# Kernel optimization log

Hardware: AMD Instinct MI355X
Metric: run time of the kernel (lower is better)

The kernel has to match this reference:

```python
import jax, jax.numpy as jnp
import numpy as np
from jax import lax

MARGIN = 0.2
NMAX = 1


def setup_inputs() -> dict:
    key = jax.random.key(0)
    k1, k2 = jax.random.split(key)
    N, D = 8192, 512
    imgs = jax.random.normal(k1, (N, D), dtype=jnp.float32)
    caps = jax.random.normal(k2, (N, D), dtype=jnp.float32)
    return {"imgs": imgs, "caps": caps}


def reference(imgs, caps):
    # scores[i, j] = <img_i, cap_j>  -> [N, N]
    scores = jnp.matmul(imgs, caps.T)
    diag = jnp.diagonal(scores)  # [N]
    s = scores - 2.0 * jnp.diag(diag)
    # top-nmax over columns (axis 0): hardest negative captions per caption slot
    max_c = lax.top_k(s.T, NMAX)[0].T  # [NMAX, N]
    # top-nmax over rows (axis 1): hardest negative images per image slot
    max_i = lax.top_k(s, NMAX)[0]      # [N, NMAX]
    neg_cap = jnp.sum(jnp.maximum(max_c + (MARGIN - diag)[None, :], 0.0))
    neg_img = jnp.sum(jnp.maximum(max_i + (MARGIN - diag)[:, None], 0.0))
    return neg_cap + neg_img
```

## Files before the change

### kernel.cpp

```cpp
#include <hip/hip_runtime.h>

#define N_ROWS 8192
#define DIM    512

typedef __attribute__((ext_vector_type(4))) float frag_cd;
typedef __attribute__((ext_vector_type(2))) long long v2ll;

__device__ __forceinline__ unsigned f2fp8(float x) {
    float a = fabsf(x);
    unsigned s = (__float_as_uint(x) >> 31) << 7;
    if (a < 0.015625f) return s;
    a = fminf(a, 448.f);
    unsigned u = __float_as_uint(a);
    u += 0x7FFFFu + ((u >> 20) & 1u);
    unsigned exp = (u >> 23) - 120u;
    unsigned mant = (u >> 20) & 7u;
    return s | (exp << 3) | mant;
}
__device__ __forceinline__ unsigned pack4fp8(float4 v) {
    return f2fp8(v.x) | (f2fp8(v.y) << 8) | (f2fp8(v.z) << 16) | (f2fp8(v.w) << 24);
}
__device__ __forceinline__ unsigned enc_f32(float f) {
    unsigned u = __float_as_uint(f);
    return (u & 0x80000000u) ? ~u : (u | 0x80000000u);
}
__device__ __forceinline__ float dec_f32(unsigned k) {
    return __uint_as_float((k & 0x80000000u) ? (k & 0x7FFFFFFFu) : ~k);
}


__global__ __launch_bounds__(256) void k_prep(const float* __restrict__ imgs,
                                              const float* __restrict__ caps,
                                              unsigned char* __restrict__ fimgs,
                                              unsigned char* __restrict__ fcaps,
                                              float* __restrict__ diag,
                                              unsigned* __restrict__ rowmax,
                                              unsigned* __restrict__ colmax,
                                              float* __restrict__ out) {
    const int cr = blockIdx.x;
    const int t  = threadIdx.x;
    const int w = t >> 6, l = t & 63;
    const int kp = l >> 3, cg = l & 3, par = (l >> 2) & 1;
    if (cr == 0 && t == 0) out[0] = 0.f;
    const size_t ubase = (size_t)cr * 8192 + kp * 1024 + cg * 256 + par * 8;
    float ps[4];
    #pragma unroll
    for (int i = 0; i < 4; ++i) {
        const int row = w + 4 * i;
        const float* ar = imgs + ((size_t)cr * 16 + row) * DIM + l * 8;
        const float* br = caps + ((size_t)cr * 16 + row) * DIM + l * 8;
        float4 a0 = *(const float4*)ar, a1 = *(const float4*)(ar + 4);
        float4 b0 = *(const float4*)br, b1 = *(const float4*)(br + 4);
        uint2 oa, ob;
        oa.x = pack4fp8(a0); oa.y = pack4fp8(a1);
        ob.x = pack4fp8(b0); ob.y = pack4fp8(b1);
        *(uint2*)(fimgs + ubase + row * 16) = oa;
        *(uint2*)(fcaps + ubase + row * 16) = ob;
        ps[i] = a0.x * b0.x + a0.y * b0.y + a0.z * b0.z + a0.w * b0.w
              + a1.x * b1.x + a1.y * b1.y + a1.z * b1.z + a1.w * b1.w;
    }
    #pragma unroll
    for (int i = 0; i < 4; ++i) {
        float s = ps[i];
        #pragma unroll
        for (int m = 1; m < 64; m <<= 1) s += __shfl_xor(s, m, 64);
        if (l == 0) {
            const int r = cr * 16 + w + 4 * i;
            diag[r] = s; rowmax[r] = 0u; colmax[r] = 0u;
        }
    }
}

__global__ __launch_bounds__(256, 6) void k_gemm(const unsigned char* __restrict__ A,
                                                 const unsigned char* __restrict__ B,
                                                 unsigned* __restrict__ rowmax,
                                                 unsigned* __restrict__ colmax) {
    __shared__ unsigned char sA[2][4096];
    __shared__ unsigned char sB[2][8192];
    const int tid = threadIdx.x;
    const int w = tid >> 6, lane = tid & 63;
    const int f = (int)blockIdx.x;
    const int jb = (f & 7) * 8 + ((f >> 3) & 7);
    const int ib = f >> 6;
    const int j0 = jb << 7, i0 = ib << 6;
    const int q = lane >> 4, l15 = lane & 15;
    const int wr = (w & 1) << 5, wc = (w >> 1) << 6;

    const unsigned char* Ab = A + (size_t)(i0 >> 4) * 8192 + lane * 16;
    const unsigned char* Bb = B + (size_t)(j0 >> 4) * 8192 + lane * 16;

    frag_cd acc[2][4] = {};

    auto stage = [&](int bi, int kp) {
        __builtin_amdgcn_global_load_lds(
            (const __attribute__((address_space(1))) unsigned int*)(Ab + (size_t)w * 8192 + kp * 1024),
            (__attribute__((address_space(3))) unsigned int*)(&sA[bi][(w << 10) + (lane << 4)]), 16, 0, 0);
        #pragma unroll
        for (int j = 0; j < 2; ++j) {
            const int s = 2 * w + j;
            __builtin_amdgcn_global_load_lds(
                (const __attribute__((address_space(1))) unsigned int*)(Bb + (size_t)s * 8192 + kp * 1024),
                (__attribute__((address_space(3))) unsigned int*)(&sB[bi][(s << 10) + (lane << 4)]), 16, 0, 0);
        }
    };

    stage(0, 0);
    __syncthreads();

    const int u16 = ((q << 4) + l15) << 4;

    #pragma unroll
    for (int kp = 0; kp < 8; ++kp) {
        const int cur = kp & 1, nxt = cur ^ 1;
        if (kp < 7) stage(nxt, kp + 1);

        v2ll af[2], bfr[4];
        #pragma unroll
        for (int r = 0; r < 2; ++r)
            af[r] = *(const v2ll*)(&sA[cur][((((w & 1) << 1) + r) << 10) + u16]);
        #pragma unroll
        for (int c = 0; c < 4; ++c)
            bfr[c] = *(const v2ll*)(&sB[cur][((((w >> 1) << 2) + c) << 10) + u16]);
        #pragma unroll
        for (int r = 0; r < 2; ++r)
            #pragma unroll
            for (int c = 0; c < 4; ++c)
                acc[r][c] = __builtin_amdgcn_mfma_f32_16x16x32_fp8_fp8(af[r][0], bfr[c][0], acc[r][c], 0, 0, 0);
        #pragma unroll
        for (int r = 0; r < 2; ++r)
            #pragma unroll
            for (int c = 0; c < 4; ++c)
                acc[r][c] = __builtin_amdgcn_mfma_f32_16x16x32_fp8_fp8(af[r][1], bfr[c][1], acc[r][c], 0, 0, 0);

        __syncthreads();
    }

    const bool dblk = ((i0 >> 7) == jb);
    #pragma unroll
    for (int r = 0; r < 2; ++r)
        #pragma unroll
        for (int c = 0; c < 4; ++c)
            #pragma unroll
            for (int g = 0; g < 4; ++g) {
                float fv = acc[r][c][g];
                const int gi = wr + (r << 4) + (q << 2) + g;
                const int gj = wc + (c << 4) + l15;
                if (dblk && (i0 + gi) == (j0 + gj)) fv = -fv;
                acc[r][c][g] = fv;
            }

    #pragma unroll
    for (int r = 0; r < 2; ++r)
        #pragma unroll
        for (int g = 0; g < 4; ++g) {
            float m = fmaxf(fmaxf(acc[r][0][g], acc[r][1][g]),
                            fmaxf(acc[r][2][g], acc[r][3][g]));
            m = fmaxf(m, __shfl_xor(m, 1, 64));
            m = fmaxf(m, __shfl_xor(m, 2, 64));
            m = fmaxf(m, __shfl_xor(m, 4, 64));
            m = fmaxf(m, __shfl_xor(m, 8, 64));
            if (l15 == 0)
                atomicMax(&rowmax[i0 + wr + (r << 4) + (q << 2) + g], enc_f32(m));
        }
    #pragma unroll
    for (int c = 0; c < 4; ++c) {
        float m = acc[0][c][0];
        #pragma unroll
        for (int r = 0; r < 2; ++r)
            #pragma unroll
            for (int g = 0; g < 4; ++g) m = fmaxf(m, acc[r][c][g]);
        m = fmaxf(m, __shfl_xor(m, 16, 64));
        m = fmaxf(m, __shfl_xor(m, 32, 64));
        if (q == 0)
            atomicMax(&colmax[j0 + wc + (c << 4) + l15], enc_f32(m));
    }
}

__global__ __launch_bounds__(256) void k_final(const unsigned* __restrict__ rowmax,
                                               const unsigned* __restrict__ colmax,
                                               const float* __restrict__ diag,
                                               float* __restrict__ out) {
    const int idx = blockIdx.x * 256 + threadIdx.x;
    const float d = diag[idx];
    float s = fmaxf(dec_f32(rowmax[idx]) + 0.2f - d, 0.f)
            + fmaxf(dec_f32(colmax[idx]) + 0.2f - d, 0.f);
    #pragma unroll
    for (int m = 1; m < 64; m <<= 1) s += __shfl_xor(s, m, 64);
    __shared__ float red[4];
    if ((threadIdx.x & 63) == 0) red[threadIdx.x >> 6] = s;
    __syncthreads();
    if (threadIdx.x == 0)
        atomicAdd(out, red[0] + red[1] + red[2] + red[3]);
}

extern "C" void kernel_launch(void* const* d_in, const int* in_sizes, int n_in,
                              void* d_out, int out_size, void* d_ws, size_t ws_size,
                              hipStream_t stream) {
    const float* imgs = (const float*)d_in[0];
    const float* caps = (const float*)d_in[1];
    float* out = (float*)d_out;

    char* ws = (char*)d_ws;
    unsigned char* fimgs = (unsigned char*)ws;
    unsigned char* fcaps = (unsigned char*)(ws + 4194304);
    float*    diag   = (float*)   (ws + 8388608);
    unsigned* rowmax = (unsigned*)(ws + 8388608 + 32768);
    unsigned* colmax = (unsigned*)(ws + 8388608 + 65536);

    k_prep<<<N_ROWS / 16, 256, 0, stream>>>(imgs, caps, fimgs, fcaps,
                                            diag, rowmax, colmax, out);
    k_gemm<<<8192, 256, 0, stream>>>(fimgs, fcaps, rowmax, colmax);
    k_final<<<N_ROWS / 256, 256, 0, stream>>>(rowmax, colmax, diag, out);
}
```

Baseline: 159.6 us.

## Switch FP8 GEMM to 16x16x128 scaled MFMA with matching operand layout

Replaces pairs of 16x16x32 fp8 MFMAs with the gfx950 16x16x128 f8f6f4 scaled MFMA using unit scales, so each step now covers 128 K. The prep kernel is rewritten to emit a packed layout matching the wider operand fragments, and it launches more blocks, each converting fewer rows. The GEMM stages double-sized LDS tiles over four K steps instead of eight, with the occupancy hint lowered to match the larger shared memory. The aims are fewer MFMA issues and sync points; the costs are more LDS per block and a likely drop in occupancy.

```diff
diff --git a/kernel.cpp b/kernel.cpp
--- a/kernel.cpp
+++ b/kernel.cpp
@@ -4,7 +4,8 @@
 #define DIM    512
 
 typedef __attribute__((ext_vector_type(4))) float frag_cd;
-typedef __attribute__((ext_vector_type(2))) long long v2ll;
+typedef __attribute__((ext_vector_type(4))) int   v4i;
+typedef __attribute__((ext_vector_type(8))) int   v8i;
 
 __device__ __forceinline__ unsigned f2fp8(float x) {
     float a = fabsf(x);
@@ -37,46 +38,38 @@
                                               unsigned* __restrict__ rowmax,
                                               unsigned* __restrict__ colmax,
                                               float* __restrict__ out) {
-    const int cr = blockIdx.x;
+    const int b  = blockIdx.x;
+    const int cr = b >> 2;
     const int t  = threadIdx.x;
     const int w = t >> 6, l = t & 63;
-    const int kp = l >> 3, cg = l & 3, par = (l >> 2) & 1;
-    if (cr == 0 && t == 0) out[0] = 0.f;
-    const size_t ubase = (size_t)cr * 8192 + kp * 1024 + cg * 256 + par * 8;
-    float ps[4];
-    #pragma unroll
-    for (int i = 0; i < 4; ++i) {
-        const int row = w + 4 * i;
-        const float* ar = imgs + ((size_t)cr * 16 + row) * DIM + l * 8;
-        const float* br = caps + ((size_t)cr * 16 + row) * DIM + l * 8;
-        float4 a0 = *(const float4*)ar, a1 = *(const float4*)(ar + 4);
-        float4 b0 = *(const float4*)br, b1 = *(const float4*)(br + 4);
-        uint2 oa, ob;
-        oa.x = pack4fp8(a0); oa.y = pack4fp8(a1);
-        ob.x = pack4fp8(b0); ob.y = pack4fp8(b1);
-        *(uint2*)(fimgs + ubase + row * 16) = oa;
-        *(uint2*)(fcaps + ubase + row * 16) = ob;
-        ps[i] = a0.x * b0.x + a0.y * b0.y + a0.z * b0.z + a0.w * b0.w
-              + a1.x * b1.x + a1.y * b1.y + a1.z * b1.z + a1.w * b1.w;
-    }
-    #pragma unroll
-    for (int i = 0; i < 4; ++i) {
-        float s = ps[i];
-        #pragma unroll
-        for (int m = 1; m < 64; m <<= 1) s += __shfl_xor(s, m, 64);
-        if (l == 0) {
-            const int r = cr * 16 + w + 4 * i;
-            diag[r] = s; rowmax[r] = 0u; colmax[r] = 0u;
-        }
-    }
-}
-
-__global__ __launch_bounds__(256, 6) void k_gemm(const unsigned char* __restrict__ A,
+    const int row = ((b & 3) << 2) + w;
+    if (b == 0 && t == 0) out[0] = 0.f;
+    const int r = cr * 16 + row;
+    const float* ar = imgs + (size_t)r * DIM + l * 8;
+    const float* br = caps + (size_t)r * DIM + l * 8;
+    float4 a0 = *(const float4*)ar, a1 = *(const float4*)(ar + 4);
+    float4 b0 = *(const float4*)br, b1 = *(const float4*)(br + 4);
+    uint2 oa, ob;
+    oa.x = pack4fp8(a0); oa.y = pack4fp8(a1);
+    ob.x = pack4fp8(b0); ob.y = pack4fp8(b1);
+    const size_t addr = (size_t)cr * 8192 + (size_t)((l >> 4) << 11)
+                      + (((l >> 1) & 1) << 10)
+                      + ((((l >> 2) & 3) << 4) + row) * 16 + ((l & 1) << 3);
+    *(uint2*)(fimgs + addr) = oa;
+    *(uint2*)(fcaps + addr) = ob;
+    float s = a0.x * b0.x + a0.y * b0.y + a0.z * b0.z + a0.w * b0.w
+            + a1.x * b1.x + a1.y * b1.y + a1.z * b1.z + a1.w * b1.w;
+    #pragma unroll
+    for (int m = 1; m < 64; m <<= 1) s += __shfl_xor(s, m, 64);
+    if (l == 0) { diag[r] = s; rowmax[r] = 0u; colmax[r] = 0u; }
+}
+
+__global__ __launch_bounds__(256, 3) void k_gemm(const unsigned char* __restrict__ A,
                                                  const unsigned char* __restrict__ B,
                                                  unsigned* __restrict__ rowmax,
                                                  unsigned* __restrict__ colmax) {
-    __shared__ unsigned char sA[2][4096];
-    __shared__ unsigned char sB[2][8192];
+    __shared__ unsigned char sA[2][8192];
+    __shared__ unsigned char sB[2][16384];
     const int tid = threadIdx.x;
     const int w = tid >> 6, lane = tid & 63;
     const int f = (int)blockIdx.x;
@@ -91,46 +84,61 @@
 
     frag_cd acc[2][4] = {};
 
-    auto stage = [&](int bi, int kp) {
-        __builtin_amdgcn_global_load_lds(
-            (const __attribute__((address_space(1))) unsigned int*)(Ab + (size_t)w * 8192 + kp * 1024),
-            (__attribute__((address_space(3))) unsigned int*)(&sA[bi][(w << 10) + (lane << 4)]), 16, 0, 0);
-        #pragma unroll
-        for (int j = 0; j < 2; ++j) {
-            const int s = 2 * w + j;
+    auto stage = [&](int bi, int kp2) {
+        #pragma unroll
+        for (int j = 0; j < 2; ++j)
             __builtin_amdgcn_global_load_lds(
-                (const __attribute__((address_space(1))) unsigned int*)(Bb + (size_t)s * 8192 + kp * 1024),
-                (__attribute__((address_space(3))) unsigned int*)(&sB[bi][(s << 10) + (lane << 4)]), 16, 0, 0);
+                (const __attribute__((address_space(1))) unsigned int*)(Ab + (size_t)w * 8192 + kp2 * 2048 + j * 1024),
+                (__attribute__((address_space(3))) unsigned int*)(&sA[bi][(w << 11) + (j << 10) + (lane << 4)]), 16, 0, 0);
+        #pragma unroll
+        for (int s = 0; s < 2; ++s) {
+            const int ch = 2 * w + s;
+            #pragma unroll
+            for (int j = 0; j < 2; ++j)
+                __builtin_amdgcn_global_load_lds(
+                    (const __attribute__((address_space(1))) unsigned int*)(Bb + (size_t)ch * 8192 + kp2 * 2048 + j * 1024),
+                    (__attribute__((address_space(3))) unsigned int*)(&sB[bi][(ch << 11) + (j << 10) + (lane << 4)]), 16, 0, 0);
         }
     };
 
     stage(0, 0);
     __syncthreads();
 
-    const int u16 = ((q << 4) + l15) << 4;
-
-    #pragma unroll
-    for (int kp = 0; kp < 8; ++kp) {
-        const int cur = kp & 1, nxt = cur ^ 1;
-        if (kp < 7) stage(nxt, kp + 1);
-
-        v2ll af[2], bfr[4];
+    const int u16 = lane << 4;
+
+    #pragma unroll
+    for (int kp2 = 0; kp2 < 4; ++kp2) {
+        const int cur = kp2 & 1, nxt = cur ^ 1;
+        if (kp2 < 3) stage(nxt, kp2 + 1);
+
+        v8i af[2], bf[4];
+        #pragma unroll
+        for (int r = 0; r < 2; ++r) {
+            const int ch = ((w & 1) << 1) + r;
+            v4i lo = *(const v4i*)(&sA[cur][(ch << 11) + u16]);
+            v4i hi = *(const v4i*)(&sA[cur][(ch << 11) + 1024 + u16]);
+            v8i v;
+            v[0] = lo[0]; v[1] = lo[1]; v[2] = lo[2]; v[3] = lo[3];
+            v[4] = hi[0]; v[5] = hi[1]; v[6] = hi[2]; v[7] = hi[3];
+            af[r] = v;
+        }
+        #pragma unroll
+        for (int c = 0; c < 4; ++c) {
+            const int ch = ((w >> 1) << 2) + c;
+            v4i lo = *(const v4i*)(&sB[cur][(ch << 11) + u16]);
+            v4i hi = *(const v4i*)(&sB[cur][(ch << 11) + 1024 + u16]);
+            v8i v;
+            v[0] = lo[0]; v[1] = lo[1]; v[2] = lo[2]; v[3] = lo[3];
+            v[4] = hi[0]; v[5] = hi[1]; v[6] = hi[2]; v[7] = hi[3];
+            bf[c] = v;
+        }
         #pragma unroll
         for (int r = 0; r < 2; ++r)
-            af[r] = *(const v2ll*)(&sA[cur][((((w & 1) << 1) + r) << 10) + u16]);
-        #pragma unroll
-        for (int c = 0; c < 4; ++c)
-            bfr[c] = *(const v2ll*)(&sB[cur][((((w >> 1) << 2) + c) << 10) + u16]);
-        #pragma unroll
-        for (int r = 0; r < 2; ++r)
             #pragma unroll
             for (int c = 0; c < 4; ++c)
-                acc[r][c] = __builtin_amdgcn_mfma_f32_16x16x32_fp8_fp8(af[r][0], bfr[c][0], acc[r][c], 0, 0, 0);
-        #pragma unroll
-        for (int r = 0; r < 2; ++r)
-            #pragma unroll
-            for (int c = 0; c < 4; ++c)
-                acc[r][c] = __builtin_amdgcn_mfma_f32_16x16x32_fp8_fp8(af[r][1], bfr[c][1], acc[r][c], 0, 0, 0);
+                acc[r][c] = __builtin_amdgcn_mfma_scale_f32_16x16x128_f8f6f4(
+                    af[r], bf[c], acc[r][c], 0, 0,
+                    0, 0x7F7F7F7F, 0, 0x7F7F7F7F);
 
         __syncthreads();
     }
@@ -207,8 +215,8 @@
     unsigned* rowmax = (unsigned*)(ws + 8388608 + 32768);
     unsigned* colmax = (unsigned*)(ws + 8388608 + 65536);
 
-    k_prep<<<N_ROWS / 16, 256, 0, stream>>>(imgs, caps, fimgs, fcaps,
-                                            diag, rowmax, colmax, out);
+    k_prep<<<2048, 256, 0, stream>>>(imgs, caps, fimgs, fcaps,
+                                     diag, rowmax, colmax, out);
     k_gemm<<<8192, 256, 0, stream>>>(fimgs, fcaps, rowmax, colmax);
     k_final<<<N_ROWS / 256, 256, 0, stream>>>(rowmax, colmax, diag, out);
 }
```

After: 191.7 us. 20.1% more time.

## Enlarge GEMM tile to 128x128 with four-stage LDS pipeline

Applied to the files above, without the earlier changes.

The fused fp8 GEMM+max kernel moves from 64x128 to 128x128 output tiles per block, so each wave computes a 64x64 sub-tile with 4x4 MFMA accumulators, halving the grid. Staging becomes a 4-deep ring buffer with three stages in flight, explicit vmcnt waits and raw barriers, plus s_setprio around the MFMA burst. The aim is more operand reuse per LDS byte and better latency hiding, at the cost of more registers and LDS, lower occupancy (launch bounds 2) and fewer blocks in the atomic epilogue.

```diff
diff --git a/kernel.cpp b/kernel.cpp
--- a/kernel.cpp
+++ b/kernel.cpp
@@ -71,73 +71,84 @@
     }
 }
 
-__global__ __launch_bounds__(256, 6) void k_gemm(const unsigned char* __restrict__ A,
+__global__ __launch_bounds__(256, 2) void k_gemm(const unsigned char* __restrict__ A,
                                                  const unsigned char* __restrict__ B,
                                                  unsigned* __restrict__ rowmax,
                                                  unsigned* __restrict__ colmax) {
-    __shared__ unsigned char sA[2][4096];
-    __shared__ unsigned char sB[2][8192];
+    __shared__ unsigned char sA[4][8192];
+    __shared__ unsigned char sB[4][8192];
     const int tid = threadIdx.x;
     const int w = tid >> 6, lane = tid & 63;
     const int f = (int)blockIdx.x;
     const int jb = (f & 7) * 8 + ((f >> 3) & 7);
     const int ib = f >> 6;
-    const int j0 = jb << 7, i0 = ib << 6;
+    const int j0 = jb << 7, i0 = ib << 7;
     const int q = lane >> 4, l15 = lane & 15;
-    const int wr = (w & 1) << 5, wc = (w >> 1) << 6;
+    const int wr = (w & 1) << 6, wc = (w >> 1) << 6;
 
     const unsigned char* Ab = A + (size_t)(i0 >> 4) * 8192 + lane * 16;
     const unsigned char* Bb = B + (size_t)(j0 >> 4) * 8192 + lane * 16;
 
-    frag_cd acc[2][4] = {};
-
-    auto stage = [&](int bi, int kp) {
-        __builtin_amdgcn_global_load_lds(
-            (const __attribute__((address_space(1))) unsigned int*)(Ab + (size_t)w * 8192 + kp * 1024),
-            (__attribute__((address_space(3))) unsigned int*)(&sA[bi][(w << 10) + (lane << 4)]), 16, 0, 0);
+    auto stage = [&](int t) {
+        const int buf = t & 3;
         #pragma unroll
         for (int j = 0; j < 2; ++j) {
-            const int s = 2 * w + j;
+            const int ch = 2 * w + j;
             __builtin_amdgcn_global_load_lds(
-                (const __attribute__((address_space(1))) unsigned int*)(Bb + (size_t)s * 8192 + kp * 1024),
-                (__attribute__((address_space(3))) unsigned int*)(&sB[bi][(s << 10) + (lane << 4)]), 16, 0, 0);
+                (const __attribute__((address_space(1))) unsigned int*)(Ab + (size_t)ch * 8192 + t * 1024),
+                (__attribute__((address_space(3))) unsigned int*)(&sA[buf][(ch << 10) + (lane << 4)]), 16, 0, 0);
+            __builtin_amdgcn_global_load_lds(
+                (const __attribute__((address_space(1))) unsigned int*)(Bb + (size_t)ch * 8192 + t * 1024),
+                (__attribute__((address_space(3))) unsigned int*)(&sB[buf][(ch << 10) + (lane << 4)]), 16, 0, 0);
         }
     };
 
-    stage(0, 0);
-    __syncthreads();
-
-    const int u16 = ((q << 4) + l15) << 4;
-
-    #pragma unroll
-    for (int kp = 0; kp < 8; ++kp) {
-        const int cur = kp & 1, nxt = cur ^ 1;
-        if (kp < 7) stage(nxt, kp + 1);
-
-        v2ll af[2], bfr[4];
-        #pragma unroll
-        for (int r = 0; r < 2; ++r)
-            af[r] = *(const v2ll*)(&sA[cur][((((w & 1) << 1) + r) << 10) + u16]);
-        #pragma unroll
-        for (int c = 0; c < 4; ++c)
-            bfr[c] = *(const v2ll*)(&sB[cur][((((w >> 1) << 2) + c) << 10) + u16]);
-        #pragma unroll
-        for (int r = 0; r < 2; ++r)
-            #pragma unroll
-            for (int c = 0; c < 4; ++c)
-                acc[r][c] = __builtin_amdgcn_mfma_f32_16x16x32_fp8_fp8(af[r][0], bfr[c][0], acc[r][c], 0, 0, 0);
-        #pragma unroll
-        for (int r = 0; r < 2; ++r)
-            #pragma unroll
-            for (int c = 0; c < 4; ++c)
-                acc[r][c] = __builtin_amdgcn_mfma_f32_16x16x32_fp8_fp8(af[r][1], bfr[c][1], acc[r][c], 0, 0, 0);
-
-        __syncthreads();
-    }
-
-    const bool dblk = ((i0 >> 7) == jb);
-    #pragma unroll
-    for (int r = 0; r < 2; ++r)
+    stage(0); stage(1); stage(2);
+    asm volatile("s_waitcnt vmcnt(8)" ::: "memory");
+    __builtin_amdgcn_s_barrier();
+    __builtin_amdgcn_sched_barrier(0);
+
+    frag_cd acc[4][4] = {};
+    const int ca0 = (w & 1) << 2, cb0 = (w >> 1) << 2;
+    const int u16 = lane << 4;
+
+    #pragma unroll
+    for (int t = 0; t < 8; ++t) {
+        if (t > 0) {
+            if (t <= 5)      asm volatile("s_waitcnt vmcnt(8) lgkmcnt(0)" ::: "memory");
+            else if (t == 6) asm volatile("s_waitcnt vmcnt(4) lgkmcnt(0)" ::: "memory");
+            else             asm volatile("s_waitcnt vmcnt(0) lgkmcnt(0)" ::: "memory");
+            __builtin_amdgcn_s_barrier();
+            __builtin_amdgcn_sched_barrier(0);
+        }
+        if (t + 3 < 8) stage(t + 3);
+
+        v2ll af[4], bf[4];
+        #pragma unroll
+        for (int m = 0; m < 4; ++m)
+            af[m] = *(const v2ll*)(&sA[t & 3][((ca0 + m) << 10) + u16]);
+        #pragma unroll
+        for (int n = 0; n < 4; ++n)
+            bf[n] = *(const v2ll*)(&sB[t & 3][((cb0 + n) << 10) + u16]);
+
+        __builtin_amdgcn_s_setprio(1);
+        #pragma unroll
+        for (int m = 0; m < 4; ++m)
+            #pragma unroll
+            for (int n = 0; n < 4; ++n)
+                acc[m][n] = __builtin_amdgcn_mfma_f32_16x16x32_fp8_fp8(af[m][0], bf[n][0], acc[m][n], 0, 0, 0);
+        #pragma unroll
+        for (int m = 0; m < 4; ++m)
+            #pragma unroll
+            for (int n = 0; n < 4; ++n)
+                acc[m][n] = __builtin_amdgcn_mfma_f32_16x16x32_fp8_fp8(af[m][1], bf[n][1], acc[m][n], 0, 0, 0);
+        __builtin_amdgcn_s_setprio(0);
+        __builtin_amdgcn_sched_barrier(0);
+    }
+
+    const bool dblk = (i0 == j0);
+    #pragma unroll
+    for (int r = 0; r < 4; ++r)
         #pragma unroll
         for (int c = 0; c < 4; ++c)
             #pragma unroll
@@ -150,7 +161,7 @@
             }
 
     #pragma unroll
-    for (int r = 0; r < 2; ++r)
+    for (int r = 0; r < 4; ++r)
         #pragma unroll
         for (int g = 0; g < 4; ++g) {
             float m = fmaxf(fmaxf(acc[r][0][g], acc[r][1][g]),
@@ -166,7 +177,7 @@
     for (int c = 0; c < 4; ++c) {
         float m = acc[0][c][0];
         #pragma unroll
-        for (int r = 0; r < 2; ++r)
+        for (int r = 0; r < 4; ++r)
             #pragma unroll
             for (int g = 0; g < 4; ++g) m = fmaxf(m, acc[r][c][g]);
         m = fmaxf(m, __shfl_xor(m, 16, 64));
@@ -209,6 +220,6 @@
 
     k_prep<<<N_ROWS / 16, 256, 0, stream>>>(imgs, caps, fimgs, fcaps,
                                             diag, rowmax, colmax, out);
-    k_gemm<<<8192, 256, 0, stream>>>(fimgs, fcaps, rowmax, colmax);
+    k_gemm<<<4096, 256, 0, stream>>>(fimgs, fcaps, rowmax, colmax);
     k_final<<<N_ROWS / 256, 256, 0, stream>>>(rowmax, colmax, diag, out);
 }
```

Result: slower. 198.3 us (+24.2%).

## Triple-buffer GEMM loads with manual waitcnt and fuse final reduction via last-block counter

Applied to the files above, without the earlier changes.

The GEMM staging moves from double to triple buffering in LDS, with a prefetch distance of two. A single barrier per k-step replaces two syncthreads, guarded by explicit vmcnt/lgkmcnt waits, and s_setprio raises priority around the MFMA block. The separate k_final launch is removed: the last block to finish, found through an atomic counter, computes the hinge-loss sum, which saves one kernel launch. Occupancy is lowered from 6 to 4 blocks per CU because LDS use grows, and the diagonal negation now runs only on diagonal blocks. The LDS fragment indexing also changes from ((q<<4)+l15)<<4 to lane<<4, which is the same value.

```diff
diff --git a/kernel.cpp b/kernel.cpp
--- a/kernel.cpp
+++ b/kernel.cpp
@@ -36,12 +36,13 @@
                                               float* __restrict__ diag,
                                               unsigned* __restrict__ rowmax,
                                               unsigned* __restrict__ colmax,
-                                              float* __restrict__ out) {
+                                              float* __restrict__ out,
+                                              unsigned* __restrict__ cnt) {
     const int cr = blockIdx.x;
     const int t  = threadIdx.x;
     const int w = t >> 6, l = t & 63;
     const int kp = l >> 3, cg = l & 3, par = (l >> 2) & 1;
-    if (cr == 0 && t == 0) out[0] = 0.f;
+    if (cr == 0 && t == 0) { out[0] = 0.f; cnt[0] = 0u; }
     const size_t ubase = (size_t)cr * 8192 + kp * 1024 + cg * 256 + par * 8;
     float ps[4];
     #pragma unroll
@@ -71,12 +72,15 @@
     }
 }
 
-__global__ __launch_bounds__(256, 6) void k_gemm(const unsigned char* __restrict__ A,
+__global__ __launch_bounds__(256, 4) void k_gemm(const unsigned char* __restrict__ A,
                                                  const unsigned char* __restrict__ B,
                                                  unsigned* __restrict__ rowmax,
-                                                 unsigned* __restrict__ colmax) {
-    __shared__ unsigned char sA[2][4096];
-    __shared__ unsigned char sB[2][8192];
+                                                 unsigned* __restrict__ colmax,
+                                                 const float* __restrict__ diag,
+                                                 float* __restrict__ out,
+                                                 unsigned* __restrict__ cnt) {
+    __shared__ unsigned char sA[3][4096];
+    __shared__ unsigned char sB[3][8192];
     const int tid = threadIdx.x;
     const int w = tid >> 6, lane = tid & 63;
     const int f = (int)blockIdx.x;
@@ -89,65 +93,68 @@
     const unsigned char* Ab = A + (size_t)(i0 >> 4) * 8192 + lane * 16;
     const unsigned char* Bb = B + (size_t)(j0 >> 4) * 8192 + lane * 16;
 
+    auto stage = [&](int t) {
+        const int buf = t % 3;
+        __builtin_amdgcn_global_load_lds(
+            (const __attribute__((address_space(1))) unsigned int*)(Ab + (size_t)w * 8192 + t * 1024),
+            (__attribute__((address_space(3))) unsigned int*)(&sA[buf][(w << 10) + (lane << 4)]), 16, 0, 0);
+        #pragma unroll
+        for (int j = 0; j < 2; ++j) {
+            const int ch = 2 * w + j;
+            __builtin_amdgcn_global_load_lds(
+                (const __attribute__((address_space(1))) unsigned int*)(Bb + (size_t)ch * 8192 + t * 1024),
+                (__attribute__((address_space(3))) unsigned int*)(&sB[buf][(ch << 10) + (lane << 4)]), 16, 0, 0);
+        }
+    };
+
+    stage(0); stage(1);
+
     frag_cd acc[2][4] = {};
-
-    auto stage = [&](int bi, int kp) {
-        __builtin_amdgcn_global_load_lds(
-            (const __attribute__((address_space(1))) unsigned int*)(Ab + (size_t)w * 8192 + kp * 1024),
-            (__attribute__((address_space(3))) unsigned int*)(&sA[bi][(w << 10) + (lane << 4)]), 16, 0, 0);
-        #pragma unroll
-        for (int j = 0; j < 2; ++j) {
-            const int s = 2 * w + j;
-            __builtin_amdgcn_global_load_lds(
-                (const __attribute__((address_space(1))) unsigned int*)(Bb + (size_t)s * 8192 + kp * 1024),
-                (__attribute__((address_space(3))) unsigned int*)(&sB[bi][(s << 10) + (lane << 4)]), 16, 0, 0);
-        }
-    };
-
-    stage(0, 0);
-    __syncthreads();
-
-    const int u16 = ((q << 4) + l15) << 4;
-
-    #pragma unroll
-    for (int kp = 0; kp < 8; ++kp) {
-        const int cur = kp & 1, nxt = cur ^ 1;
-        if (kp < 7) stage(nxt, kp + 1);
-
-        v2ll af[2], bfr[4];
-        #pragma unroll
-        for (int r = 0; r < 2; ++r)
-            af[r] = *(const v2ll*)(&sA[cur][((((w & 1) << 1) + r) << 10) + u16]);
+    const int u16 = lane << 4;
+
+    #pragma unroll
+    for (int t = 0; t < 8; ++t) {
+        if (t == 0)      asm volatile("s_waitcnt vmcnt(3)" ::: "memory");
+        else if (t < 7)  asm volatile("s_waitcnt vmcnt(3) lgkmcnt(0)" ::: "memory");
+        else             asm volatile("s_waitcnt vmcnt(0) lgkmcnt(0)" ::: "memory");
+        __builtin_amdgcn_s_barrier();
+        if (t + 2 < 8) stage(t + 2);
+
+        v2ll af[2], bf[4];
+        #pragma unroll
+        for (int r = 0; r < 2; ++r)
+            af[r] = *(const v2ll*)(&sA[t % 3][((((w & 1) << 1) + r) << 10) + u16]);
         #pragma unroll
         for (int c = 0; c < 4; ++c)
-            bfr[c] = *(const v2ll*)(&sB[cur][((((w >> 1) << 2) + c) << 10) + u16]);
+            bf[c] = *(const v2ll*)(&sB[t % 3][((((w >> 1) << 2) + c) << 10) + u16]);
+
+        __builtin_amdgcn_s_setprio(1);
         #pragma unroll
         for (int r = 0; r < 2; ++r)
             #pragma unroll
             for (int c = 0; c < 4; ++c)
-                acc[r][c] = __builtin_amdgcn_mfma_f32_16x16x32_fp8_fp8(af[r][0], bfr[c][0], acc[r][c], 0, 0, 0);
+                acc[r][c] = __builtin_amdgcn_mfma_f32_16x16x32_fp8_fp8(af[r][0], bf[c][0], acc[r][c], 0, 0, 0);
         #pragma unroll
         for (int r = 0; r < 2; ++r)
             #pragma unroll
             for (int c = 0; c < 4; ++c)
-                acc[r][c] = __builtin_amdgcn_mfma_f32_16x16x32_fp8_fp8(af[r][1], bfr[c][1], acc[r][c], 0, 0, 0);
-
-        __syncthreads();
+                acc[r][c] = __builtin_amdgcn_mfma_f32_16x16x32_fp8_fp8(af[r][1], bf[c][1], acc[r][c], 0, 0, 0);
+        __builtin_amdgcn_s_setprio(0);
     }
 
     const bool dblk = ((i0 >> 7) == jb);
-    #pragma unroll
-    for (int r = 0; r < 2; ++r)
-        #pragma unroll
-        for (int c = 0; c < 4; ++c)
-            #pragma unroll
-            for (int g = 0; g < 4; ++g) {
-                float fv = acc[r][c][g];
-                const int gi = wr + (r << 4) + (q << 2) + g;
-                const int gj = wc + (c << 4) + l15;
-                if (dblk && (i0 + gi) == (j0 + gj)) fv = -fv;
-                acc[r][c][g] = fv;
-            }
+    if (dblk) {
+        #pragma unroll
+        for (int r = 0; r < 2; ++r)
+            #pragma unroll
+            for (int c = 0; c < 4; ++c)
+                #pragma unroll
+                for (int g = 0; g < 4; ++g) {
+                    const int gi = wr + (r << 4) + (q << 2) + g;
+                    const int gj = wc + (c << 4) + l15;
+                    if ((i0 + gi) == (j0 + gj)) acc[r][c][g] = -acc[r][c][g];
+                }
+    }
 
     #pragma unroll
     for (int r = 0; r < 2; ++r)
@@ -174,23 +181,31 @@
         if (q == 0)
             atomicMax(&colmax[j0 + wc + (c << 4) + l15], enc_f32(m));
     }
-}
-
-__global__ __launch_bounds__(256) void k_final(const unsigned* __restrict__ rowmax,
-                                               const unsigned* __restrict__ colmax,
-                                               const float* __restrict__ diag,
-                                               float* __restrict__ out) {
-    const int idx = blockIdx.x * 256 + threadIdx.x;
-    const float d = diag[idx];
-    float s = fmaxf(dec_f32(rowmax[idx]) + 0.2f - d, 0.f)
-            + fmaxf(dec_f32(colmax[idx]) + 0.2f - d, 0.f);
-    #pragma unroll
-    for (int m = 1; m < 64; m <<= 1) s += __shfl_xor(s, m, 64);
-    __shared__ float red[4];
-    if ((threadIdx.x & 63) == 0) red[threadIdx.x >> 6] = s;
+
+    __shared__ unsigned sDone;
     __syncthreads();
-    if (threadIdx.x == 0)
-        atomicAdd(out, red[0] + red[1] + red[2] + red[3]);
+    if (tid == 0) {
+        __threadfence();
+        sDone = (atomicAdd(cnt, 1u) == 8191u) ? 1u : 0u;
+    }
+    __syncthreads();
+    if (sDone) {
+        float s = 0.f;
+        const int base = tid * 32;
+        #pragma unroll 4
+        for (int k = 0; k < 32; ++k) {
+            const int idx = base + k;
+            const float d = diag[idx];
+            s += fmaxf(dec_f32(atomicMax(&rowmax[idx], 0u)) + 0.2f - d, 0.f)
+               + fmaxf(dec_f32(atomicMax(&colmax[idx], 0u)) + 0.2f - d, 0.f);
+        }
+        #pragma unroll
+        for (int m = 1; m < 64; m <<= 1) s += __shfl_xor(s, m, 64);
+        __shared__ float red[4];
+        if ((tid & 63) == 0) red[tid >> 6] = s;
+        __syncthreads();
+        if (tid == 0) out[0] = red[0] + red[1] + red[2] + red[3];
+    }
 }
 
 extern "C" void kernel_launch(void* const* d_in, const int* in_sizes, int n_in,
@@ -206,9 +221,9 @@
     float*    diag   = (float*)   (ws + 8388608);
     unsigned* rowmax = (unsigned*)(ws + 8388608 + 32768);
     unsigned* colmax = (unsigned*)(ws + 8388608 + 65536);
+    unsigned* cnt    = (unsigned*)(ws + 8388608 + 98304);
 
     k_prep<<<N_ROWS / 16, 256, 0, stream>>>(imgs, caps, fimgs, fcaps,
-                                            diag, rowmax, colmax, out);
-    k_gemm<<<8192, 256, 0, stream>>>(fimgs, fcaps, rowmax, colmax);
-    k_final<<<N_ROWS / 256, 256, 0, stream>>>(rowmax, colmax, diag, out);
-}
+                                            diag, rowmax, colmax, out, cnt);
+    k_gemm<<<8192, 256, 0, stream>>>(fimgs, fcaps, rowmax, colmax, diag, out, cnt);
+}
```

New measurement: 301.6 us. 88.9% more time.
